# Kernel optimization log

Hardware: AMD Instinct MI355X
Metric: run time of the kernel (lower is better)

Reference implementation:

```python
import jax, jax.numpy as jnp
import numpy as np

N_NODES = 100000
N_EDGES = 1600000
IN_FEA, HIDDEN, RANK = 128, 128, 64


def setup_inputs() -> dict:
    key = jax.random.key(0)
    ks = jax.random.split(key, 6)
    stdv = 1.0 / np.sqrt(HIDDEN)  # reset_parameters uses 1/sqrt(V.size(0)) = 1/sqrt(hidden)
    return {
        "x": jax.random.normal(ks[0], (N_NODES, IN_FEA), dtype=jnp.float32),
        "norm": jax.random.uniform(ks[1], (N_NODES, 1), dtype=jnp.float32),
        "W": jax.random.uniform(ks[2], (IN_FEA, RANK), minval=-stdv, maxval=stdv, dtype=jnp.float32),
        "V": jax.random.uniform(ks[3], (HIDDEN, RANK), minval=-stdv, maxval=stdv, dtype=jnp.float32),
        "src": jax.random.randint(ks[4], (N_EDGES,), 0, N_NODES, dtype=jnp.int32),
        "dst": jax.random.randint(ks[5], (N_EDGES,), 0, N_NODES, dtype=jnp.int32),
    }


def _segment_prod(m, seg, num_segments):
    # product-reduce over ragged mailboxes via sign/log decomposition
    # (numerically equivalent to prod, differentiable: d prod / d m_i = prod / m_i)
    logp = jax.ops.segment_sum(jnp.log(jnp.abs(m)), seg, num_segments=num_segments)
    n_neg = jax.ops.segment_sum((m < 0).astype(m.dtype), seg, num_segments=num_segments)
    sign = 1.0 - 2.0 * jnp.mod(n_neg, 2.0)
    # nodes with no in-edges get logp=0, sign=1 -> product identity 1
    return sign * jnp.exp(logp)


def reference(x, norm, W, V, src, dst):
    n = x.shape[0]
    h = x @ W                      # [N, rank] linear projection
    m = h[src]                     # [E, rank] gather messages along edges
    neigh = _segment_prod(m, dst, n)   # [N, rank] elementwise-product aggregation
    trans_x = norm * neigh         # [N, rank]
    return trans_x @ V.T           # [N, hidden]
```

## Files before the change

### kernel.cpp

```cpp
#include <hip/hip_runtime.h>
#include <hip/hip_bf16.h>

#define N_NODES 100000
#define N_EDGES 1600000
#define IN_FEA 128
#define HIDDEN 128
#define RANK 64

#define NBUCK 391
#define C_BLOCKS 1024
#define EPB 1563
#define S_BLOCKS 128
#define CHUNK_W (EPB * 8)
#define GEMM1_BLOCKS 1563


__device__ __forceinline__ void fma4(float4& a, float s, const float4& b) {
    a.x = fmaf(s, b.x, a.x);
    a.y = fmaf(s, b.y, a.y);
    a.z = fmaf(s, b.z, a.z);
    a.w = fmaf(s, b.w, a.w);
}

__device__ __forceinline__ unsigned short f2bf_rne(float f) {
    unsigned u = __float_as_uint(f);
    u += 0x7fffu + ((u >> 16) & 1u);
    return (unsigned short)(u >> 16);
}

__device__ __forceinline__ float bf2f(unsigned short s) {
    return __uint_as_float(((unsigned)s) << 16);
}

__device__ __forceinline__ float bfu_lo(unsigned u) {
    return __uint_as_float(u << 16);
}
__device__ __forceinline__ float bfu_hi(unsigned u) {
    return __uint_as_float(u & 0xffff0000u);
}


__global__ __launch_bounds__(256) void gemm1_hist_kernel(const float* __restrict__ x,
                                                         const float* __restrict__ W,
                                                         unsigned short* __restrict__ hb,
                                                         const int* __restrict__ dst,
                                                         int* __restrict__ bhist,
                                                         int* __restrict__ blockhist) {
    __shared__ float Wl[IN_FEA * RANK];
    int t = threadIdx.x;

    if (blockIdx.x >= GEMM1_BLOCKS) {
        int* hist = (int*)Wl;
        int b = blockIdx.x - GEMM1_BLOCKS;
        for (int i = t; i < NBUCK; i += 256) hist[i] = 0;
        __syncthreads();
        int b0 = b * EPB;
        int b1 = min(b0 + EPB, N_EDGES);
        for (int e = b0 + t; e < b1; e += 256)
            atomicAdd(&hist[dst[e] >> 8], 1);
        __syncthreads();
        for (int i = t; i < NBUCK; i += 256) {
            int c = hist[i];
            blockhist[b * NBUCK + i] = c;
            if (c) atomicAdd(&bhist[i], c);
        }
        return;
    }

    for (int i = t; i < IN_FEA * RANK; i += 256) Wl[i] = W[i];
    __syncthreads();

    int r0 = (t & 15) * 4;
    int n0 = blockIdx.x * 64 + (t >> 4) * 4;
    const float4* x0 = (const float4*)(x + (long)min(n0 + 0, N_NODES - 1) * IN_FEA);
    const float4* x1 = (const float4*)(x + (long)min(n0 + 1, N_NODES - 1) * IN_FEA);
    const float4* x2 = (const float4*)(x + (long)min(n0 + 2, N_NODES - 1) * IN_FEA);
    const float4* x3 = (const float4*)(x + (long)min(n0 + 3, N_NODES - 1) * IN_FEA);
    float4 a0 = {0.f, 0.f, 0.f, 0.f}, a1 = a0, a2 = a0, a3 = a0;
    for (int k4 = 0; k4 < IN_FEA / 4; ++k4) {
        float4 v0 = x0[k4], v1 = x1[k4], v2 = x2[k4], v3 = x3[k4];
        int kb = k4 * 4;
        float4 w0 = *(const float4*)&Wl[(kb + 0) * RANK + r0];
        float4 w1 = *(const float4*)&Wl[(kb + 1) * RANK + r0];
        float4 w2 = *(const float4*)&Wl[(kb + 2) * RANK + r0];
        float4 w3 = *(const float4*)&Wl[(kb + 3) * RANK + r0];
        fma4(a0, v0.x, w0); fma4(a0, v0.y, w1); fma4(a0, v0.z, w2); fma4(a0, v0.w, w3);
        fma4(a1, v1.x, w0); fma4(a1, v1.y, w1); fma4(a1, v1.z, w2); fma4(a1, v1.w, w3);
        fma4(a2, v2.x, w0); fma4(a2, v2.y, w1); fma4(a2, v2.z, w2); fma4(a2, v2.w, w3);
        fma4(a3, v3.x, w0); fma4(a3, v3.y, w1); fma4(a3, v3.z, w2); fma4(a3, v3.w, w3);
    }
    float4 accs[4] = {a0, a1, a2, a3};
#pragma unroll
    for (int i = 0; i < 4; ++i) {
        if (n0 + i < N_NODES) {
            ushort4 o;
            o.x = f2bf_rne(accs[i].x); o.y = f2bf_rne(accs[i].y);
            o.z = f2bf_rne(accs[i].z); o.w = f2bf_rne(accs[i].w);
            *(ushort4*)(hb + (n0 + i) * RANK + r0) = o;
        }
    }
}


__global__ void bucket_scan_kernel(const int* __restrict__ bhist,
                                   int* __restrict__ bucket_offs,
                                   int* __restrict__ bucket_cursor,
                                   int* __restrict__ offs) {
    __shared__ int sd[512];
    int t = threadIdx.x;
    int v = (t < NBUCK) ? bhist[t] : 0;
    sd[t] = v;
    __syncthreads();
    for (int off = 1; off < 512; off <<= 1) {
        int a = 0;
        if (t >= off) a = sd[t - off];
        __syncthreads();
        sd[t] += a;
        __syncthreads();
    }
    if (t < NBUCK) {
        int excl = sd[t] - v;
        bucket_offs[t] = excl;
        bucket_cursor[t] = excl;
    }
    if (t == 0) {
        bucket_offs[NBUCK] = N_EDGES;
        offs[N_NODES] = N_EDGES;
    }
}

__global__ __launch_bounds__(1024) void binscatter_kernel(const int* __restrict__ src,
                                                          const int* __restrict__ dst,
                                                          const int* __restrict__ blockhist,
                                                          int* __restrict__ bucket_cursor,
                                                          unsigned* __restrict__ pairs) {
    __shared__ int wbase[NBUCK];
    __shared__ int cur[NBUCK];
    int t = threadIdx.x;
    int b = blockIdx.x;
    if (t < NBUCK) {
        int s = 0;
#pragma unroll
        for (int k = 0; k < 8; ++k)
            s += blockhist[(8 * b + k) * NBUCK + t];
        wbase[t] = s ? atomicAdd(&bucket_cursor[t], s) : 0;
        cur[t] = 0;
    }
    __syncthreads();
    int e0 = b * CHUNK_W;
    int e1 = min(e0 + CHUNK_W, N_EDGES);
    for (int e = e0 + t; e < e1; e += 1024) {
        int d = dst[e];
        int s = src[e];
        int bk = d >> 8;
        int lp = atomicAdd(&cur[bk], 1);
        pairs[wbase[bk] + lp] = ((unsigned)s << 8) | (unsigned)(d & 255);
    }
}

__global__ __launch_bounds__(256) void bucket_build_kernel(const unsigned* __restrict__ pairs,
                                                           const int* __restrict__ bucket_offs,
                                                           int* __restrict__ offs,
                                                           int* __restrict__ eidx) {
    __shared__ int dcnt[256];
    __shared__ int sd[256];
    __shared__ int cur[256];
    int b = blockIdx.x, t = threadIdx.x;
    int base = bucket_offs[b], end = bucket_offs[b + 1];
    dcnt[t] = 0;
    __syncthreads();
    for (int i = base + t; i < end; i += 256)
        atomicAdd(&dcnt[pairs[i] & 255u], 1);
    __syncthreads();
    int v = dcnt[t];
    sd[t] = v;
    __syncthreads();
    for (int off = 1; off < 256; off <<= 1) {
        int a = 0;
        if (t >= off) a = sd[t - off];
        __syncthreads();
        sd[t] += a;
        __syncthreads();
    }
    int excl = sd[t] - v;
    int node = b * 256 + t;
    if (node < N_NODES) offs[node] = base + excl;
    cur[t] = excl;
    __syncthreads();
    for (int i = base + t; i < end; i += 256) {
        unsigned r = pairs[i];
        int lp = atomicAdd(&cur[r & 255u], 1);
        eidx[base + lp] = (int)(r >> 8);
    }
}


__global__ __launch_bounds__(1024) void agg_gemm_kernel(const unsigned short* __restrict__ hb,
                                                        const float* __restrict__ norm,
                                                        const float* __restrict__ V,
                                                        const int* __restrict__ offs,
                                                        const int* __restrict__ eidx,
                                                        float* __restrict__ out) {
    __shared__ float VL[HIDDEN * 68];
    __shared__ float pls[16][64];
    int t = threadIdx.x;
    {
        const float4* V4 = (const float4*)V;
#pragma unroll
        for (int k = 0; k < 2; ++k) {
            int i4 = t + 1024 * k;
            float4 v = V4[i4];
            int el = i4 << 2;
            *(float4*)&VL[(el >> 6) * 68 + (el & 63)] = v;
        }
    }
    __syncthreads();

    int wave = t >> 6, lane = t & 63;
    int half = lane >> 5;
    int l32 = lane & 31;
    int node = blockIdx.x * 16 + wave;
    int beg = offs[node], end = offs[node + 1];
    const unsigned* hb2 = (const unsigned*)hb;

    float plo = 1.0f, phi = 1.0f;
    for (int c = beg; c < end; c += 64) {
        int n = min(64, end - c);
        int sidx = (c + lane < end) ? eidx[c + lane] : 0;
        int j = 0;
        for (; j + 16 <= n; j += 16) {
            int s0 = __shfl(sidx, j + 0  + half);
            int s1 = __shfl(sidx, j + 2  + half);
            int s2 = __shfl(sidx, j + 4  + half);
            int s3 = __shfl(sidx, j + 6  + half);
            int s4 = __shfl(sidx, j + 8  + half);
            int s5 = __shfl(sidx, j + 10 + half);
            int s6 = __shfl(sidx, j + 12 + half);
            int s7 = __shfl(sidx, j + 14 + half);
            unsigned u0 = hb2[(s0 << 5) | l32];
            unsigned u1 = hb2[(s1 << 5) | l32];
            unsigned u2 = hb2[(s2 << 5) | l32];
            unsigned u3 = hb2[(s3 << 5) | l32];
            unsigned u4 = hb2[(s4 << 5) | l32];
            unsigned u5 = hb2[(s5 << 5) | l32];
            unsigned u6 = hb2[(s6 << 5) | l32];
            unsigned u7 = hb2[(s7 << 5) | l32];
            plo *= ((bfu_lo(u0) * bfu_lo(u1)) * (bfu_lo(u2) * bfu_lo(u3))) *
                   ((bfu_lo(u4) * bfu_lo(u5)) * (bfu_lo(u6) * bfu_lo(u7)));
            phi *= ((bfu_hi(u0) * bfu_hi(u1)) * (bfu_hi(u2) * bfu_hi(u3))) *
                   ((bfu_hi(u4) * bfu_hi(u5)) * (bfu_hi(u6) * bfu_hi(u7)));
        }
        for (; j + 8 <= n; j += 8) {
            int s0 = __shfl(sidx, j + 0 + half);
            int s1 = __shfl(sidx, j + 2 + half);
            int s2 = __shfl(sidx, j + 4 + half);
            int s3 = __shfl(sidx, j + 6 + half);
            unsigned u0 = hb2[(s0 << 5) | l32];
            unsigned u1 = hb2[(s1 << 5) | l32];
            unsigned u2 = hb2[(s2 << 5) | l32];
            unsigned u3 = hb2[(s3 << 5) | l32];
            plo *= (bfu_lo(u0) * bfu_lo(u1)) * (bfu_lo(u2) * bfu_lo(u3));
            phi *= (bfu_hi(u0) * bfu_hi(u1)) * (bfu_hi(u2) * bfu_hi(u3));
        }
        for (; j < n; j += 2) {
            int jj = j + half;
            int s = __shfl(sidx, jj);
            unsigned u = hb2[(s << 5) | l32];
            float alo = bfu_lo(u), ahi = bfu_hi(u);
            if (jj >= n) { alo = 1.0f; ahi = 1.0f; }
            plo *= alo;
            phi *= ahi;
        }
    }
    plo *= __shfl_xor(plo, 32);
    phi *= __shfl_xor(phi, 32);

    if (lane < 32) {
        float nrm = norm[node];
        float2 o;
        o.x = plo * nrm;
        o.y = phi * nrm;
        *(float2*)&pls[wave][l32 * 2] = o;
    }

    const float4* pw = (const float4*)pls[wave];
    const float4* rA = (const float4*)&VL[lane * 68];
    const float4* rB = (const float4*)&VL[(lane + 64) * 68];
    float accA = 0.f, accB = 0.f;
#pragma unroll
    for (int q = 0; q < 16; ++q) {
        float4 pp = pw[q];
        float4 va = rA[q];
        float4 vb = rB[q];
        accA = fmaf(pp.x, va.x, fmaf(pp.y, va.y, fmaf(pp.z, va.z, fmaf(pp.w, va.w, accA))));
        accB = fmaf(pp.x, vb.x, fmaf(pp.y, vb.y, fmaf(pp.z, vb.z, fmaf(pp.w, vb.w, accB))));
    }
    out[node * HIDDEN + lane]      = accA;
    out[node * HIDDEN + 64 + lane] = accB;
}


extern "C" void kernel_launch(void* const* d_in, const int* in_sizes, int n_in,
                              void* d_out, int out_size, void* d_ws, size_t ws_size,
                              hipStream_t stream) {
    const float* x    = (const float*)d_in[0];
    const float* norm = (const float*)d_in[1];
    const float* W    = (const float*)d_in[2];
    const float* V    = (const float*)d_in[3];
    const int*   src  = (const int*)d_in[4];
    const int*   dst  = (const int*)d_in[5];
    float* out = (float*)d_out;

    unsigned short* hb = (unsigned short*)d_ws;
    int*   offs        = (int*)(hb + (long)N_NODES * RANK);
    int*   eidx        = offs + N_NODES + 1;
    int*   bhist       = eidx + N_EDGES;
    int*   bucket_offs = bhist + NBUCK;
    int*   bucket_cur  = bucket_offs + NBUCK + 1;

    unsigned* pairs    = (unsigned*)d_out;
    int*     blockhist = (int*)d_out + 2097152;

    hipMemsetAsync(bhist, 0, NBUCK * sizeof(int), stream);
    gemm1_hist_kernel<<<GEMM1_BLOCKS + C_BLOCKS, 256, 0, stream>>>(x, W, hb, dst, bhist, blockhist);
    bucket_scan_kernel<<<1, 512, 0, stream>>>(bhist, bucket_offs, bucket_cur, offs);
    binscatter_kernel<<<S_BLOCKS, 1024, 0, stream>>>(src, dst, blockhist, bucket_cur, pairs);
    bucket_build_kernel<<<NBUCK, 256, 0, stream>>>(pairs, bucket_offs, offs, eidx);
    agg_gemm_kernel<<<N_NODES / 16, 1024, 0, stream>>>(hb, norm, V, offs, eidx, out);
}
```

Before: 264.8 us.

## Batch 64 nodes per block in aggregation, register-tiled V GEMM with staged stores

```diff
diff --git a/kernel.cpp b/kernel.cpp
--- a/kernel.cpp
+++ b/kernel.cpp
@@ -14,6 +14,8 @@
 #define CHUNK_W (EPB * 8)
 #define GEMM1_BLOCKS 1563
 
+#define AGG_BLOCKS 1563
+
 
 __device__ __forceinline__ void fma4(float4& a, float s, const float4& b) {
     a.x = fmaf(s, b.x, a.x);
@@ -26,10 +28,6 @@
     unsigned u = __float_as_uint(f);
     u += 0x7fffu + ((u >> 16) & 1u);
     return (unsigned short)(u >> 16);
-}
-
-__device__ __forceinline__ float bf2f(unsigned short s) {
-    return __uint_as_float(((unsigned)s) << 16);
 }
 
 __device__ __forceinline__ float bfu_lo(unsigned u) {
@@ -195,108 +193,129 @@
 }
 
 
-__global__ __launch_bounds__(1024) void agg_gemm_kernel(const unsigned short* __restrict__ hb,
-                                                        const float* __restrict__ norm,
-                                                        const float* __restrict__ V,
-                                                        const int* __restrict__ offs,
-                                                        const int* __restrict__ eidx,
-                                                        float* __restrict__ out) {
-    __shared__ float VL[HIDDEN * 68];
-    __shared__ float pls[16][64];
+__global__ __launch_bounds__(512, 4) void agg_gemm_kernel(const unsigned short* __restrict__ hb,
+                                                          const float* __restrict__ norm,
+                                                          const float* __restrict__ V,
+                                                          const int* __restrict__ offs,
+                                                          const int* __restrict__ eidx,
+                                                          float* __restrict__ out) {
+    __shared__ float pls[64 * 68];
+    __shared__ float outbuf[64 * 132];
     int t = threadIdx.x;
-    {
-        const float4* V4 = (const float4*)V;
-#pragma unroll
-        for (int k = 0; k < 2; ++k) {
-            int i4 = t + 1024 * k;
-            float4 v = V4[i4];
-            int el = i4 << 2;
-            *(float4*)&VL[(el >> 6) * 68 + (el & 63)] = v;
-        }
-    }
-    __syncthreads();
-
-    int wave = t >> 6, lane = t & 63;
+    int w = t >> 6, lane = t & 63;
     int half = lane >> 5;
     int l32 = lane & 31;
-    int node = blockIdx.x * 16 + wave;
-    int beg = offs[node], end = offs[node + 1];
+    int base = blockIdx.x * 64;
     const unsigned* hb2 = (const unsigned*)hb;
 
-    float plo = 1.0f, phi = 1.0f;
-    for (int c = beg; c < end; c += 64) {
-        int n = min(64, end - c);
-        int sidx = (c + lane < end) ? eidx[c + lane] : 0;
-        int j = 0;
-        for (; j + 16 <= n; j += 16) {
-            int s0 = __shfl(sidx, j + 0  + half);
-            int s1 = __shfl(sidx, j + 2  + half);
-            int s2 = __shfl(sidx, j + 4  + half);
-            int s3 = __shfl(sidx, j + 6  + half);
-            int s4 = __shfl(sidx, j + 8  + half);
-            int s5 = __shfl(sidx, j + 10 + half);
-            int s6 = __shfl(sidx, j + 12 + half);
-            int s7 = __shfl(sidx, j + 14 + half);
-            unsigned u0 = hb2[(s0 << 5) | l32];
-            unsigned u1 = hb2[(s1 << 5) | l32];
-            unsigned u2 = hb2[(s2 << 5) | l32];
-            unsigned u3 = hb2[(s3 << 5) | l32];
-            unsigned u4 = hb2[(s4 << 5) | l32];
-            unsigned u5 = hb2[(s5 << 5) | l32];
-            unsigned u6 = hb2[(s6 << 5) | l32];
-            unsigned u7 = hb2[(s7 << 5) | l32];
-            plo *= ((bfu_lo(u0) * bfu_lo(u1)) * (bfu_lo(u2) * bfu_lo(u3))) *
-                   ((bfu_lo(u4) * bfu_lo(u5)) * (bfu_lo(u6) * bfu_lo(u7)));
-            phi *= ((bfu_hi(u0) * bfu_hi(u1)) * (bfu_hi(u2) * bfu_hi(u3))) *
-                   ((bfu_hi(u4) * bfu_hi(u5)) * (bfu_hi(u6) * bfu_hi(u7)));
-        }
-        for (; j + 8 <= n; j += 8) {
-            int s0 = __shfl(sidx, j + 0 + half);
-            int s1 = __shfl(sidx, j + 2 + half);
-            int s2 = __shfl(sidx, j + 4 + half);
-            int s3 = __shfl(sidx, j + 6 + half);
-            unsigned u0 = hb2[(s0 << 5) | l32];
-            unsigned u1 = hb2[(s1 << 5) | l32];
-            unsigned u2 = hb2[(s2 << 5) | l32];
-            unsigned u3 = hb2[(s3 << 5) | l32];
-            plo *= (bfu_lo(u0) * bfu_lo(u1)) * (bfu_lo(u2) * bfu_lo(u3));
-            phi *= (bfu_hi(u0) * bfu_hi(u1)) * (bfu_hi(u2) * bfu_hi(u3));
-        }
-        for (; j < n; j += 2) {
-            int jj = j + half;
-            int s = __shfl(sidx, jj);
-            unsigned u = hb2[(s << 5) | l32];
-            float alo = bfu_lo(u), ahi = bfu_hi(u);
-            if (jj >= n) { alo = 1.0f; ahi = 1.0f; }
-            plo *= alo;
-            phi *= ahi;
-        }
-    }
-    plo *= __shfl_xor(plo, 32);
-    phi *= __shfl_xor(phi, 32);
-
-    if (lane < 32) {
-        float nrm = norm[node];
-        float2 o;
-        o.x = plo * nrm;
-        o.y = phi * nrm;
-        *(float2*)&pls[wave][l32 * 2] = o;
-    }
-
-    const float4* pw = (const float4*)pls[wave];
-    const float4* rA = (const float4*)&VL[lane * 68];
-    const float4* rB = (const float4*)&VL[(lane + 64) * 68];
-    float accA = 0.f, accB = 0.f;
-#pragma unroll
-    for (int q = 0; q < 16; ++q) {
-        float4 pp = pw[q];
-        float4 va = rA[q];
-        float4 vb = rB[q];
-        accA = fmaf(pp.x, va.x, fmaf(pp.y, va.y, fmaf(pp.z, va.z, fmaf(pp.w, va.w, accA))));
-        accB = fmaf(pp.x, vb.x, fmaf(pp.y, vb.y, fmaf(pp.z, vb.z, fmaf(pp.w, vb.w, accB))));
-    }
-    out[node * HIDDEN + lane]      = accA;
-    out[node * HIDDEN + 64 + lane] = accB;
+#pragma clang loop unroll(disable)
+    for (int i = 0; i < 8; ++i) {
+        int node = base + w * 8 + i;
+        int beg = 0, end = 0;
+        if (node < N_NODES) { beg = offs[node]; end = offs[node + 1]; }
+
+        float plo = 1.0f, phi = 1.0f;
+        for (int c = beg; c < end; c += 64) {
+            int n = min(64, end - c);
+            int sidx = (c + lane < end) ? eidx[c + lane] : 0;
+            int j = 0;
+            for (; j + 16 <= n; j += 16) {
+                int s0 = __shfl(sidx, j + 0  + half);
+                int s1 = __shfl(sidx, j + 2  + half);
+                int s2 = __shfl(sidx, j + 4  + half);
+                int s3 = __shfl(sidx, j + 6  + half);
+                int s4 = __shfl(sidx, j + 8  + half);
+                int s5 = __shfl(sidx, j + 10 + half);
+                int s6 = __shfl(sidx, j + 12 + half);
+                int s7 = __shfl(sidx, j + 14 + half);
+                unsigned u0 = hb2[(s0 << 5) | l32];
+                unsigned u1 = hb2[(s1 << 5) | l32];
+                unsigned u2 = hb2[(s2 << 5) | l32];
+                unsigned u3 = hb2[(s3 << 5) | l32];
+                unsigned u4 = hb2[(s4 << 5) | l32];
+                unsigned u5 = hb2[(s5 << 5) | l32];
+                unsigned u6 = hb2[(s6 << 5) | l32];
+                unsigned u7 = hb2[(s7 << 5) | l32];
+                plo *= ((bfu_lo(u0) * bfu_lo(u1)) * (bfu_lo(u2) * bfu_lo(u3))) *
+                       ((bfu_lo(u4) * bfu_lo(u5)) * (bfu_lo(u6) * bfu_lo(u7)));
+                phi *= ((bfu_hi(u0) * bfu_hi(u1)) * (bfu_hi(u2) * bfu_hi(u3))) *
+                       ((bfu_hi(u4) * bfu_hi(u5)) * (bfu_hi(u6) * bfu_hi(u7)));
+            }
+            for (; j + 8 <= n; j += 8) {
+                int s0 = __shfl(sidx, j + 0 + half);
+                int s1 = __shfl(sidx, j + 2 + half);
+                int s2 = __shfl(sidx, j + 4 + half);
+                int s3 = __shfl(sidx, j + 6 + half);
+                unsigned u0 = hb2[(s0 << 5) | l32];
+                unsigned u1 = hb2[(s1 << 5) | l32];
+                unsigned u2 = hb2[(s2 << 5) | l32];
+                unsigned u3 = hb2[(s3 << 5) | l32];
+                plo *= (bfu_lo(u0) * bfu_lo(u1)) * (bfu_lo(u2) * bfu_lo(u3));
+                phi *= (bfu_hi(u0) * bfu_hi(u1)) * (bfu_hi(u2) * bfu_hi(u3));
+            }
+            for (; j < n; j += 2) {
+                int jj = j + half;
+                int s = __shfl(sidx, jj);
+                unsigned u = hb2[(s << 5) | l32];
+                float alo = bfu_lo(u), ahi = bfu_hi(u);
+                if (jj >= n) { alo = 1.0f; ahi = 1.0f; }
+                plo *= alo;
+                phi *= ahi;
+            }
+        }
+        plo *= __shfl_xor(plo, 32);
+        phi *= __shfl_xor(phi, 32);
+
+        if (lane < 32) {
+            float nrm = (node < N_NODES) ? norm[node] : 0.f;
+            float2 o;
+            o.x = plo * nrm;
+            o.y = phi * nrm;
+            *(float2*)&pls[(w * 8 + i) * 68 + l32 * 2] = o;
+        }
+        __builtin_amdgcn_sched_barrier(0);
+    }
+    __syncthreads();
+
+    float4 p4[16];
+#pragma unroll
+    for (int q = 0; q < 16; ++q)
+        p4[q] = *(const float4*)&pls[lane * 68 + q * 4];
+
+    int w_u = __builtin_amdgcn_readfirstlane(w);
+    const float* Vw = V + w_u * 16 * RANK;
+    float acc[16];
+#pragma unroll
+    for (int h0 = 0; h0 < 16; ++h0) {
+        const float* Vh = Vw + h0 * RANK;
+        float ax = 0.f, ay = 0.f, az = 0.f, aw = 0.f;
+#pragma unroll
+        for (int q = 0; q < 16; ++q) {
+            ax = fmaf(Vh[4 * q + 0], p4[q].x, ax);
+            ay = fmaf(Vh[4 * q + 1], p4[q].y, ay);
+            az = fmaf(Vh[4 * q + 2], p4[q].z, az);
+            aw = fmaf(Vh[4 * q + 3], p4[q].w, aw);
+        }
+        acc[h0] = (ax + ay) + (az + aw);
+    }
+
+#pragma unroll
+    for (int k = 0; k < 4; ++k) {
+        float4 o = {acc[4 * k + 0], acc[4 * k + 1], acc[4 * k + 2], acc[4 * k + 3]};
+        *(float4*)&outbuf[lane * 132 + w * 16 + 4 * k] = o;
+    }
+    __syncthreads();
+#pragma unroll
+    for (int m = 0; m < 4; ++m) {
+        int idx4 = m * 512 + t;
+        int row = idx4 >> 5;
+        int col4 = idx4 & 31;
+        int node = base + row;
+        if (node < N_NODES) {
+            float4 v = *(const float4*)&outbuf[row * 132 + col4 * 4];
+            *(float4*)&out[node * HIDDEN + col4 * 4] = v;
+        }
+    }
 }
 
 
@@ -326,5 +345,5 @@
     bucket_scan_kernel<<<1, 512, 0, stream>>>(bhist, bucket_offs, bucket_cur, offs);
     binscatter_kernel<<<S_BLOCKS, 1024, 0, stream>>>(src, dst, blockhist, bucket_cur, pairs);
     bucket_build_kernel<<<NBUCK, 256, 0, stream>>>(pairs, bucket_offs, offs, eidx);
-    agg_gemm_kernel<<<N_NODES / 16, 1024, 0, stream>>>(hb, norm, V, offs, eidx, out);
-}
+    agg_gemm_kernel<<<AGG_BLOCKS, 512, 0, stream>>>(hb, norm, V, offs, eidx, out);
+}
```

New measurement: 321.0 us. 1.21x slower.

## Split aggregation and output GEMM into separate kernels with register-held V

Applied to the files above, without the earlier changes.

```diff
diff --git a/kernel.cpp b/kernel.cpp
--- a/kernel.cpp
+++ b/kernel.cpp
@@ -14,6 +14,10 @@
 #define CHUNK_W (EPB * 8)
 #define GEMM1_BLOCKS 1563
 
+#define AGG_BLOCKS 6250
+#define G2_BLOCKS 1250
+#define G2_NPW 20
+
 
 __device__ __forceinline__ void fma4(float4& a, float s, const float4& b) {
     a.x = fmaf(s, b.x, a.x);
@@ -26,10 +30,6 @@
     unsigned u = __float_as_uint(f);
     u += 0x7fffu + ((u >> 16) & 1u);
     return (unsigned short)(u >> 16);
-}
-
-__device__ __forceinline__ float bf2f(unsigned short s) {
-    return __uint_as_float(((unsigned)s) << 16);
 }
 
 __device__ __forceinline__ float bfu_lo(unsigned u) {
@@ -195,27 +195,12 @@
 }
 
 
-__global__ __launch_bounds__(1024) void agg_gemm_kernel(const unsigned short* __restrict__ hb,
-                                                        const float* __restrict__ norm,
-                                                        const float* __restrict__ V,
-                                                        const int* __restrict__ offs,
-                                                        const int* __restrict__ eidx,
-                                                        float* __restrict__ out) {
-    __shared__ float VL[HIDDEN * 68];
-    __shared__ float pls[16][64];
+__global__ __launch_bounds__(1024) void agg_kernel(const unsigned short* __restrict__ hb,
+                                                   const float* __restrict__ norm,
+                                                   const int* __restrict__ offs,
+                                                   const int* __restrict__ eidx,
+                                                   float* __restrict__ out) {
     int t = threadIdx.x;
-    {
-        const float4* V4 = (const float4*)V;
-#pragma unroll
-        for (int k = 0; k < 2; ++k) {
-            int i4 = t + 1024 * k;
-            float4 v = V4[i4];
-            int el = i4 << 2;
-            *(float4*)&VL[(el >> 6) * 68 + (el & 63)] = v;
-        }
-    }
-    __syncthreads();
-
     int wave = t >> 6, lane = t & 63;
     int half = lane >> 5;
     int l32 = lane & 31;
@@ -280,23 +265,46 @@
         float2 o;
         o.x = plo * nrm;
         o.y = phi * nrm;
-        *(float2*)&pls[wave][l32 * 2] = o;
-    }
-
-    const float4* pw = (const float4*)pls[wave];
-    const float4* rA = (const float4*)&VL[lane * 68];
-    const float4* rB = (const float4*)&VL[(lane + 64) * 68];
-    float accA = 0.f, accB = 0.f;
+        *(float2*)&out[(long)node * HIDDEN + l32 * 2] = o;
+    }
+}
+
+
+__global__ __launch_bounds__(256) void gemm2_kernel(const float* __restrict__ V,
+                                                    float* __restrict__ out) {
+    int t = threadIdx.x, w = t >> 6, lane = t & 63;
+
+    float4 va[16], vb[16];
+    const float4* Va = (const float4*)(V + lane * RANK);
+    const float4* Vb = (const float4*)(V + (lane + 64) * RANK);
 #pragma unroll
-    for (int q = 0; q < 16; ++q) {
-        float4 pp = pw[q];
-        float4 va = rA[q];
-        float4 vb = rB[q];
-        accA = fmaf(pp.x, va.x, fmaf(pp.y, va.y, fmaf(pp.z, va.z, fmaf(pp.w, va.w, accA))));
-        accB = fmaf(pp.x, vb.x, fmaf(pp.y, vb.y, fmaf(pp.z, vb.z, fmaf(pp.w, vb.w, accB))));
-    }
-    out[node * HIDDEN + lane]      = accA;
-    out[node * HIDDEN + 64 + lane] = accB;
+    for (int q = 0; q < 16; ++q) { va[q] = Va[q]; vb[q] = Vb[q]; }
+
+    int wid = __builtin_amdgcn_readfirstlane(blockIdx.x * 4 + w);
+    int n0 = wid * G2_NPW;
+#pragma clang loop unroll(disable)
+    for (int i = 0; i < G2_NPW; ++i) {
+        int node = n0 + i;
+        const float* pn = out + (long)node * HIDDEN;
+        float a0 = 0.f, a1 = 0.f;
+#pragma unroll
+        for (int q = 0; q < 16; ++q) {
+            float p0 = pn[4 * q + 0];
+            float p1 = pn[4 * q + 1];
+            float p2 = pn[4 * q + 2];
+            float p3 = pn[4 * q + 3];
+            a0 = fmaf(p0, va[q].x, a0);
+            a1 = fmaf(p0, vb[q].x, a1);
+            a0 = fmaf(p1, va[q].y, a0);
+            a1 = fmaf(p1, vb[q].y, a1);
+            a0 = fmaf(p2, va[q].z, a0);
+            a1 = fmaf(p2, vb[q].z, a1);
+            a0 = fmaf(p3, va[q].w, a0);
+            a1 = fmaf(p3, vb[q].w, a1);
+        }
+        out[(long)node * HIDDEN + lane]      = a0;
+        out[(long)node * HIDDEN + 64 + lane] = a1;
+    }
 }
 
 
@@ -326,5 +334,6 @@
     bucket_scan_kernel<<<1, 512, 0, stream>>>(bhist, bucket_offs, bucket_cur, offs);
     binscatter_kernel<<<S_BLOCKS, 1024, 0, stream>>>(src, dst, blockhist, bucket_cur, pairs);
     bucket_build_kernel<<<NBUCK, 256, 0, stream>>>(pairs, bucket_offs, offs, eidx);
-    agg_gemm_kernel<<<N_NODES / 16, 1024, 0, stream>>>(hb, norm, V, offs, eidx, out);
-}
+    agg_kernel<<<AGG_BLOCKS, 1024, 0, stream>>>(hb, norm, offs, eidx, out);
+    gemm2_kernel<<<G2_BLOCKS, 256, 0, stream>>>(V, out);
+}
```

After: 309.6 us. 1.17x slower.
